# Performance work log

Hardware: AMD Instinct MI355X
Metric: run time of the kernel (lower is better)

Reference implementation:

```python
import jax, jax.numpy as jnp
import numpy as np
from jax.ops import segment_sum

N_NODES = 100000
N_EDGES = 3200000
N_GRAPHS = 64


def gcn_conv(x, src, dst, W, b, num_nodes):
    h = x @ W  # [N, H]
    loop = jnp.arange(num_nodes, dtype=src.dtype)
    s = jnp.concatenate([src, loop])
    d = jnp.concatenate([dst, loop])
    deg = segment_sum(jnp.ones_like(d, dtype=h.dtype), d, num_segments=num_nodes)
    dinv = jnp.where(deg > 0, jax.lax.rsqrt(deg), 0.0)
    norm = dinv[s] * dinv[d]  # [E+N]
    msgs = h[s] * norm[:, None]  # gather + scale
    out = segment_sum(msgs, d, num_segments=num_nodes)  # scatter-add to targets
    return out + b


def setup_inputs() -> dict:
    key = jax.random.key(0)
    ks = jax.random.split(key, 8)
    F_IN, H, C = 128, 256, 2
    x = jax.random.normal(ks[0], (N_NODES, F_IN), dtype=jnp.float32)
    edge_index = jax.random.randint(ks[1], (2, N_EDGES), 0, N_NODES, dtype=jnp.int64)
    batch = jnp.sort(jax.random.randint(ks[2], (N_NODES,), 0, N_GRAPHS, dtype=jnp.int64))
    W1 = jax.random.normal(ks[3], (F_IN, H), dtype=jnp.float32) / np.sqrt(F_IN)
    b1 = jnp.zeros((H,), dtype=jnp.float32)
    W2 = jax.random.normal(ks[4], (H, H), dtype=jnp.float32) / np.sqrt(H)
    b2 = jnp.zeros((H,), dtype=jnp.float32)
    fc_w = jax.random.normal(ks[5], (H, C), dtype=jnp.float32) / np.sqrt(H)
    fc_b = jnp.zeros((C,), dtype=jnp.float32)
    return {"x": x, "edge_index": edge_index, "batch": batch, "W1": W1, "b1": b1,
            "W2": W2, "b2": b2, "fc_w": fc_w, "fc_b": fc_b}


def reference(x, edge_index, batch, W1, b1, W2, b2, fc_w, fc_b):
    src, dst = edge_index[0], edge_index[1]
    n = x.shape[0]
    h = jax.nn.relu(gcn_conv(x, src, dst, W1, b1, n))
    h = jax.nn.relu(gcn_conv(h, src, dst, W2, b2, n))
    # global_mean_pool over graph ids
    sums = segment_sum(h, batch, num_segments=N_GRAPHS)  # [G, H]
    cnts = segment_sum(jnp.ones((n,), dtype=h.dtype), batch, num_segments=N_GRAPHS)
    pooled = sums / jnp.maximum(cnts, 1.0)[:, None]
    logits = pooled @ fc_w + fc_b
    return jax.nn.log_softmax(logits, axis=1)
```

## Files before the change

### kernel.cpp

```cpp
#include <hip/hip_runtime.h>
#include <cstdint>

#define N_NODES 100000
#define N_EDGES 3200000
#define N_GRAPHS 64
#define HDIM 256
#define F_IN 128

#define BUCKET_BITS 7
#define NPB 128
#define N_BUCKETS ((N_NODES + NPB - 1) / NPB)
#define CHUNK 8192
#define NCHUNK ((N_EDGES + CHUNK - 1) / CHUNK)

typedef __attribute__((ext_vector_type(8))) short bf16x8;
typedef __attribute__((ext_vector_type(4))) float f32x4;
typedef __attribute__((ext_vector_type(2))) float f32x2;

__device__ __forceinline__ unsigned short f2bf(float f) {
    unsigned int b = __float_as_uint(f);
    b = (b + 0x7FFFu + ((b >> 16) & 1u)) >> 16;
    return (unsigned short)b;
}
__device__ __forceinline__ float bf2f(unsigned short u) {
    return __uint_as_float((unsigned int)u << 16);
}

__device__ __forceinline__ unsigned int pack4_fp8(float a, float b, float c, float d) {
    int v = 0;
    v = __builtin_amdgcn_cvt_pk_fp8_f32(a, b, v, false);
    v = __builtin_amdgcn_cvt_pk_fp8_f32(c, d, v, true);
    return (unsigned int)v;
}
__device__ __forceinline__ unsigned char pack1_fp8(float a) {
    int v = __builtin_amdgcn_cvt_pk_fp8_f32(a, a, 0, false);
    return (unsigned char)(v & 0xFF);
}

__global__ void zero_f(float* p, int n) {
    int i = blockIdx.x * blockDim.x + threadIdx.x;
    if (i < n) p[i] = 0.0f;
}

__global__ __launch_bounds__(256) void block_count(const int* __restrict__ dst,
                                                   int* __restrict__ counts, int nE) {
    __shared__ int hist[N_BUCKETS];
    int blk = blockIdx.x, t = threadIdx.x;
    for (int i = t; i < N_BUCKETS; i += 256) hist[i] = 0;
    __syncthreads();
    int lo = blk * CHUNK;
    int hi = lo + CHUNK < nE ? lo + CHUNK : nE;
    for (int i = lo + t; i < hi; i += 256) atomicAdd(&hist[dst[i] >> BUCKET_BITS], 1);
    __syncthreads();
    for (int i = t; i < N_BUCKETS; i += 256) counts[blk * N_BUCKETS + i] = hist[i];
}

__global__ __launch_bounds__(256) void bucket_totals(const int* __restrict__ counts,
                                                     int* __restrict__ tot) {
    __shared__ int red[256];
    int b = blockIdx.x, t = threadIdx.x;
    int s = 0;
    for (int blk = t; blk < NCHUNK; blk += 256) s += counts[blk * N_BUCKETS + b];
    red[t] = s;
    __syncthreads();
    for (int o = 128; o > 0; o >>= 1) {
        if (t < o) red[t] += red[t + o];
        __syncthreads();
    }
    if (t == 0) tot[b] = red[0];
}

__global__ __launch_bounds__(1024) void scan_buckets(const int* __restrict__ tot,
                                                     int* __restrict__ base, int nb) {
    __shared__ int lds[1024];
    int t = threadIdx.x;
    int v = (t < nb) ? tot[t] : 0;
    lds[t] = v;
    __syncthreads();
    for (int off = 1; off < 1024; off <<= 1) {
        int a = (t >= off) ? lds[t - off] : 0;
        __syncthreads();
        lds[t] += a;
        __syncthreads();
    }
    int excl = lds[t] - v;
    if (t < nb) base[t] = excl;
    if (t == nb) base[t] = excl;
}

__global__ __launch_bounds__(512) void column_scan(const int* __restrict__ counts,
                                                   const int* __restrict__ base,
                                                   int* __restrict__ offs) {
    __shared__ int lds[512];
    int b = blockIdx.x, t = threadIdx.x;
    int v = (t < NCHUNK) ? counts[t * N_BUCKETS + b] : 0;
    lds[t] = v;
    __syncthreads();
    for (int off = 1; off < 512; off <<= 1) {
        int a = (t >= off) ? lds[t - off] : 0;
        __syncthreads();
        lds[t] += a;
        __syncthreads();
    }
    if (t < NCHUNK) offs[t * N_BUCKETS + b] = base[b] + lds[t] - v;
}

__global__ __launch_bounds__(256) void block_scatter(const int* __restrict__ src,
                                                     const int* __restrict__ dst,
                                                     const int* __restrict__ offs,
                                                     unsigned int* __restrict__ rec, int nE) {
    __shared__ int cur[N_BUCKETS];
    int blk = blockIdx.x, t = threadIdx.x;
    for (int i = t; i < N_BUCKETS; i += 256) cur[i] = offs[blk * N_BUCKETS + i];
    __syncthreads();
    int lo = blk * CHUNK;
    int hi = lo + CHUNK < nE ? lo + CHUNK : nE;
    for (int i = lo + t; i < hi; i += 256) {
        int d = dst[i];
        int b = d >> BUCKET_BITS;
        int pos = atomicAdd(&cur[b], 1);
        rec[pos] = (unsigned int)src[i] | ((unsigned int)(d & (NPB - 1)) << 17);
    }
}

__global__ __launch_bounds__(512) void bucket_csr(const unsigned int* __restrict__ rec,
                                                  const int* __restrict__ base,
                                                  int* __restrict__ ptr, float* __restrict__ dinv,
                                                  int* __restrict__ csr_src, int n) {
    __shared__ int hist[NPB];
    __shared__ int sc[NPB];
    __shared__ int cur[NPB];
    int b = blockIdx.x;
    int lo = base[b], hi = base[b + 1];
    int t = threadIdx.x;
    if (t < NPB) hist[t] = 0;
    __syncthreads();
    for (int i = lo + t; i < hi; i += 512) atomicAdd(&hist[rec[i] >> 17], 1);
    __syncthreads();
    if (t < NPB) sc[t] = hist[t];
    __syncthreads();
    for (int off = 1; off < NPB; off <<= 1) {
        int a = (t < NPB && t >= off) ? sc[t - off] : 0;
        __syncthreads();
        if (t < NPB) sc[t] += a;
        __syncthreads();
    }
    if (t < NPB) {
        int node = b * NPB + t;
        int incl = sc[t];
        int excl = incl - hist[t];
        if (node < n) {
            ptr[node] = lo + incl;
            dinv[node] = rsqrtf((float)hist[t] + 1.0f);
        }
        cur[t] = lo + excl;
    }
    __syncthreads();
    for (int i = lo + t; i < hi; i += 512) {
        unsigned int r = rec[i];
        int pos = atomicAdd(&cur[r >> 17], 1);
        csr_src[pos] = (int)(r & 0x1FFFFu);
    }
}

__global__ void convert_x_pre(const float* __restrict__ x, const float* __restrict__ dinv,
                              unsigned int* __restrict__ xp, int n) {
    int tid = blockIdx.x * blockDim.x + threadIdx.x;
    if (tid >= n * (F_IN / 4)) return;
    int node = tid / (F_IN / 4);
    float di = dinv[node];
    float4 v = ((const float4*)x)[tid];
    xp[tid] = pack4_fp8(v.x * di, v.y * di, v.z * di, v.w * di);
}

__global__ void pack_w(const float* __restrict__ W, unsigned short* __restrict__ hi,
                       unsigned short* __restrict__ lo, int K) {
    int idx = blockIdx.x * blockDim.x + threadIdx.x;
    if (idx >= K * HDIM) return;
    int k = idx >> 8, c = idx & 255;
    float w = W[idx];
    unsigned short h = f2bf(w);
    float hf = __uint_as_float((unsigned int)h << 16);
    unsigned short l = f2bf(w - hf);
    int pos = ((k >> 5) * 16 + (c >> 4)) * 512 + ((((k >> 3) & 3) * 16) + (c & 15)) * 8 + (k & 7);
    hi[pos] = h;
    lo[pos] = l;
}

__global__ void csr_agg128_fp8(const unsigned char* __restrict__ h, const int* __restrict__ ptr,
                               const int* __restrict__ csr, const float* __restrict__ dinv,
                               unsigned short* __restrict__ out, int n) {
    int wave = threadIdx.x >> 6, lane = threadIdx.x & 63;
    int node = blockIdx.x * 4 + wave;
    if (node >= n) return;
    int begin = node ? ptr[node - 1] : 0;
    int end = ptr[node];
    unsigned int u = *(const unsigned short*)(h + (size_t)node * 128 + lane * 2);
    f32x2 a01 = __builtin_amdgcn_cvt_pk_f32_fp8((int)u, false);
    int i = begin;
    for (; i + 16 <= end; i += 16) {
        unsigned int uu[16];
#pragma unroll
        for (int j = 0; j < 16; j++) {
            int s = csr[i + j];
            uu[j] = *(const unsigned short*)(h + (size_t)s * 128 + lane * 2);
        }
#pragma unroll
        for (int j = 0; j < 16; j++)
            a01 += __builtin_amdgcn_cvt_pk_f32_fp8((int)uu[j], false);
    }
    for (; i + 4 <= end; i += 4) {
        unsigned int uu[4];
#pragma unroll
        for (int j = 0; j < 4; j++) {
            int s = csr[i + j];
            uu[j] = *(const unsigned short*)(h + (size_t)s * 128 + lane * 2);
        }
#pragma unroll
        for (int j = 0; j < 4; j++)
            a01 += __builtin_amdgcn_cvt_pk_f32_fp8((int)uu[j], false);
    }
    for (; i < end; i++) {
        int s = csr[i];
        unsigned int u0 = *(const unsigned short*)(h + (size_t)s * 128 + lane * 2);
        a01 += __builtin_amdgcn_cvt_pk_f32_fp8((int)u0, false);
    }
    float dn = dinv[node];
    unsigned int o = (unsigned int)f2bf(a01.x * dn) | ((unsigned int)f2bf(a01.y * dn) << 16);
    *(unsigned int*)(out + (size_t)node * 128 + lane * 2) = o;
}

__global__ void csr_agg256_fp8(const unsigned char* __restrict__ h, const int* __restrict__ ptr,
                               const int* __restrict__ csr, const float* __restrict__ dinv,
                               unsigned short* __restrict__ out, int n) {
    int wave = threadIdx.x >> 6, lane = threadIdx.x & 63;
    int node = blockIdx.x * 4 + wave;
    if (node >= n) return;
    int begin = node ? ptr[node - 1] : 0;
    int end = ptr[node];
    unsigned int u = *(const unsigned int*)(h + (size_t)node * 256 + lane * 4);
    f32x2 a01 = __builtin_amdgcn_cvt_pk_f32_fp8((int)u, false);
    f32x2 a23 = __builtin_amdgcn_cvt_pk_f32_fp8((int)u, true);
    int i = begin;
    for (; i + 16 <= end; i += 16) {
        unsigned int uu[16];
#pragma unroll
        for (int j = 0; j < 16; j++) {
            int s = csr[i + j];
            uu[j] = *(const unsigned int*)(h + (size_t)s * 256 + lane * 4);
        }
#pragma unroll
        for (int j = 0; j < 16; j++) {
            a01 += __builtin_amdgcn_cvt_pk_f32_fp8((int)uu[j], false);
            a23 += __builtin_amdgcn_cvt_pk_f32_fp8((int)uu[j], true);
        }
    }
    for (; i + 4 <= end; i += 4) {
        unsigned int uu[4];
#pragma unroll
        for (int j = 0; j < 4; j++) {
            int s = csr[i + j];
            uu[j] = *(const unsigned int*)(h + (size_t)s * 256 + lane * 4);
        }
#pragma unroll
        for (int j = 0; j < 4; j++) {
            a01 += __builtin_amdgcn_cvt_pk_f32_fp8((int)uu[j], false);
            a23 += __builtin_amdgcn_cvt_pk_f32_fp8((int)uu[j], true);
        }
    }
    for (; i < end; i++) {
        int s = csr[i];
        unsigned int u0 = *(const unsigned int*)(h + (size_t)s * 256 + lane * 4);
        a01 += __builtin_amdgcn_cvt_pk_f32_fp8((int)u0, false);
        a23 += __builtin_amdgcn_cvt_pk_f32_fp8((int)u0, true);
    }
    float dn = dinv[node];
    uint2 o;
    o.x = (unsigned int)f2bf(a01.x * dn) | ((unsigned int)f2bf(a01.y * dn) << 16);
    o.y = (unsigned int)f2bf(a23.x * dn) | ((unsigned int)f2bf(a23.y * dn) << 16);
    *(uint2*)(out + (size_t)node * 256 + lane * 4) = o;
}

template <int K, int MODE>
__global__ __launch_bounds__(256, 3) void gemm_mfma(
    const unsigned short* __restrict__ A, const unsigned short* __restrict__ Whi,
    const unsigned short* __restrict__ Wlo, const float* __restrict__ bias,
    const float* __restrict__ dinv, void* __restrict__ outp, int n) {
    int wave = threadIdx.x >> 6, lane = threadIdx.x & 63;
    int quad = lane >> 4, l16 = lane & 15;
    int rowgrp = wave >> 1, colhalf = wave & 1;
    int rowbase = blockIdx.x * 64 + rowgrp * 32;

    f32x4 acc[2][8];
#pragma unroll
    for (int s = 0; s < 2; s++)
#pragma unroll
        for (int ct = 0; ct < 8; ct++) acc[s][ct] = (f32x4){0.f, 0.f, 0.f, 0.f};

    int r0 = rowbase + l16;
    int r1 = rowbase + 16 + l16;
    int rc0 = r0 < n ? r0 : n - 1;
    int rc1 = r1 < n ? r1 : n - 1;

    for (int kt = 0; kt < K / 32; kt++) {
        bf16x8 a0 = *(const bf16x8*)(A + (size_t)rc0 * K + kt * 32 + quad * 8);
        bf16x8 a1 = *(const bf16x8*)(A + (size_t)rc1 * K + kt * 32 + quad * 8);
        const unsigned short* wh = Whi + ((size_t)kt * 16 + colhalf * 8) * 512 + lane * 8;
        const unsigned short* wl = Wlo + ((size_t)kt * 16 + colhalf * 8) * 512 + lane * 8;
#pragma unroll
        for (int ct = 0; ct < 8; ct++) {
            bf16x8 bh = *(const bf16x8*)(wh + ct * 512);
            bf16x8 bl = *(const bf16x8*)(wl + ct * 512);
            acc[0][ct] = __builtin_amdgcn_mfma_f32_16x16x32_bf16(a0, bh, acc[0][ct], 0, 0, 0);
            acc[0][ct] = __builtin_amdgcn_mfma_f32_16x16x32_bf16(a0, bl, acc[0][ct], 0, 0, 0);
            acc[1][ct] = __builtin_amdgcn_mfma_f32_16x16x32_bf16(a1, bh, acc[1][ct], 0, 0, 0);
            acc[1][ct] = __builtin_amdgcn_mfma_f32_16x16x32_bf16(a1, bl, acc[1][ct], 0, 0, 0);
        }
    }

#pragma unroll
    for (int s = 0; s < 2; s++) {
#pragma unroll
        for (int ct = 0; ct < 8; ct++) {
            int col = colhalf * 128 + ct * 16 + l16;
            float b = bias[col];
#pragma unroll
            for (int r = 0; r < 4; r++) {
                int row = rowbase + s * 16 + quad * 4 + r;
                if (row < n) {
                    float v = acc[s][ct][r] + b;
                    v = v > 0.0f ? v : 0.0f;
                    if (MODE == 0) {
                        ((unsigned char*)outp)[(size_t)row * HDIM + col] = pack1_fp8(v * dinv[row]);
                    } else {
                        ((unsigned short*)outp)[(size_t)row * HDIM + col] = f2bf(v);
                    }
                }
            }
        }
    }
}

__global__ void pool_sum_runs(const unsigned short* __restrict__ h, const int* __restrict__ batch,
                              float* __restrict__ pool, int n) {
    constexpr int ROWS = 128;
    int f = threadIdx.x;
    int r0 = blockIdx.x * ROWS;
    int rend = r0 + ROWS;
    if (rend > n) rend = n;
    float acc = 0.0f;
    int cur = batch[r0];
    for (int r = r0; r < rend; r++) {
        int g = batch[r];
        if (g != cur) {
            atomicAdd(&pool[cur * HDIM + f], acc);
            acc = 0.0f; cur = g;
        }
        acc += bf2f(h[(size_t)r * HDIM + f]);
    }
    atomicAdd(&pool[cur * HDIM + f], acc);
}

__global__ void final_head(const float* __restrict__ pool, const int* __restrict__ batch,
                           const float* __restrict__ fcw, const float* __restrict__ fcb,
                           float* __restrict__ out, int n) {
    int g = threadIdx.x;
    if (g < N_GRAPHS) {
        int lo = 0, hi = n;
        while (lo < hi) { int m = (lo + hi) >> 1; if (batch[m] < g) lo = m + 1; else hi = m; }
        int b0 = lo;
        lo = 0; hi = n;
        while (lo < hi) { int m = (lo + hi) >> 1; if (batch[m] < g + 1) lo = m + 1; else hi = m; }
        int c = lo - b0;
        float cf = c > 1 ? (float)c : 1.0f;
        float inv = 1.0f / cf;
        float l0 = fcb[0], l1 = fcb[1];
        for (int f = 0; f < HDIM; f++) {
            float p = pool[g * HDIM + f] * inv;
            l0 += p * fcw[f * 2 + 0];
            l1 += p * fcw[f * 2 + 1];
        }
        float m = fmaxf(l0, l1);
        float lse = m + logf(expf(l0 - m) + expf(l1 - m));
        out[g * 2 + 0] = l0 - lse;
        out[g * 2 + 1] = l1 - lse;
    }
}

extern "C" void kernel_launch(void* const* d_in, const int* in_sizes, int n_in,
                              void* d_out, int out_size, void* d_ws, size_t ws_size,
                              hipStream_t stream) {
    const float* x = (const float*)d_in[0];
    const int* ei = (const int*)d_in[1];
    const int* batch = (const int*)d_in[2];
    const float* W1 = (const float*)d_in[3];
    const float* b1 = (const float*)d_in[4];
    const float* W2 = (const float*)d_in[5];
    const float* b2 = (const float*)d_in[6];
    const float* fcw = (const float*)d_in[7];
    const float* fcb = (const float*)d_in[8];
    float* out = (float*)d_out;

    const int* src = ei;
    const int* dst = ei + N_EDGES;

    char* ws = (char*)d_ws;
    float* dinv = (float*)ws;            ws += 4 * ((N_NODES + 255) & ~255);
    int* ptr = (int*)ws;                 ws += 4 * ((N_NODES + 255) & ~255);
    int* csr_src = (int*)ws;             ws += 4 * (size_t)N_EDGES;
    int* counts = (int*)ws;              ws += 4 * (size_t)NCHUNK * N_BUCKETS;
    int* offs = (int*)ws;                ws += 4 * (size_t)NCHUNK * N_BUCKETS;
    int* tot = (int*)ws;                 ws += 4 * 1024;
    int* bbase = (int*)ws;               ws += 4 * 1024;
    unsigned short* W1hi = (unsigned short*)ws; ws += 2 * F_IN * HDIM;
    unsigned short* W1lo = (unsigned short*)ws; ws += 2 * F_IN * HDIM;
    unsigned short* W2hi = (unsigned short*)ws; ws += 2 * HDIM * HDIM;
    unsigned short* W2lo = (unsigned short*)ws; ws += 2 * HDIM * HDIM;
    float* pool = (float*)ws;            ws += 4 * N_GRAPHS * HDIM;
    char* R0 = ws;                       ws += 4 * (size_t)N_NODES * HDIM;
    unsigned char* x_pre = (unsigned char*)R0;
    unsigned short* A1 = (unsigned short*)(R0 + (size_t)N_NODES * F_IN);
    unsigned char* h1_pre = (unsigned char*)(R0 + 3 * (size_t)N_NODES * F_IN);
    unsigned short* h2 = (unsigned short*)R0;
    unsigned short* A2 = (unsigned short*)ws;
    unsigned int* records = (unsigned int*)A2;

    block_count<<<NCHUNK, 256, 0, stream>>>(dst, counts, N_EDGES);
    bucket_totals<<<N_BUCKETS, 256, 0, stream>>>(counts, tot);
    scan_buckets<<<1, 1024, 0, stream>>>(tot, bbase, N_BUCKETS);
    column_scan<<<N_BUCKETS, 512, 0, stream>>>(counts, bbase, offs);
    block_scatter<<<NCHUNK, 256, 0, stream>>>(src, dst, offs, records, N_EDGES);
    bucket_csr<<<N_BUCKETS, 512, 0, stream>>>(records, bbase, ptr, dinv, csr_src, N_NODES);

    convert_x_pre<<<(N_NODES * (F_IN / 4) + 255) / 256, 256, 0, stream>>>(
        x, dinv, (unsigned int*)x_pre, N_NODES);
    pack_w<<<(F_IN * HDIM + 255) / 256, 256, 0, stream>>>(W1, W1hi, W1lo, F_IN);
    pack_w<<<(HDIM * HDIM + 255) / 256, 256, 0, stream>>>(W2, W2hi, W2lo, HDIM);
    zero_f<<<(N_GRAPHS * HDIM + 255) / 256, 256, 0, stream>>>(pool, N_GRAPHS * HDIM);

    csr_agg128_fp8<<<(N_NODES + 3) / 4, 256, 0, stream>>>(x_pre, ptr, csr_src, dinv, A1, N_NODES);
    gemm_mfma<F_IN, 0><<<(N_NODES + 63) / 64, 256, 0, stream>>>(A1, W1hi, W1lo, b1, dinv,
                                                                h1_pre, N_NODES);
    csr_agg256_fp8<<<(N_NODES + 3) / 4, 256, 0, stream>>>(h1_pre, ptr, csr_src, dinv, A2, N_NODES);
    gemm_mfma<HDIM, 2><<<(N_NODES + 63) / 64, 256, 0, stream>>>(A2, W2hi, W2lo, b2, dinv,
                                                                h2, N_NODES);

    pool_sum_runs<<<(N_NODES + 127) / 128, 256, 0, stream>>>(h2, batch, pool, N_NODES);
    final_head<<<1, 64, 0, stream>>>(pool, batch, fcw, fcb, out, N_NODES);
}
```

Baseline: 650.8 us.

## Slice CSR aggregation by feature columns with edge-parallel lanes and shuffle reduce

```diff
diff --git a/kernel.cpp b/kernel.cpp
--- a/kernel.cpp
+++ b/kernel.cpp
@@ -187,80 +187,43 @@
     lo[pos] = l;
 }
 
-__global__ void csr_agg128_fp8(const unsigned char* __restrict__ h, const int* __restrict__ ptr,
-                               const int* __restrict__ csr, const float* __restrict__ dinv,
-                               unsigned short* __restrict__ out, int n) {
+template <int F>
+__global__ __launch_bounds__(256) void csr_agg_sliced(
+    const unsigned char* __restrict__ h, const int* __restrict__ ptr,
+    const int* __restrict__ csr, const float* __restrict__ dinv,
+    unsigned short* __restrict__ out, int n) {
+    constexpr int NSLICES = F / 32;
+    constexpr int NODEGRP = 8 / NSLICES;
+    int slot = blockIdx.x & 7;
+    int nodeblk = blockIdx.x >> 3;
     int wave = threadIdx.x >> 6, lane = threadIdx.x & 63;
-    int node = blockIdx.x * 4 + wave;
+    int slice = slot % NSLICES;
+    int grp = slot / NSLICES;
+    int node = nodeblk * (4 * NODEGRP) + grp * 4 + wave;
     if (node >= n) return;
+    int eg = lane >> 3;
+    int cp = lane & 7;
+    int colbyte = slice * 32 + cp * 4;
+
     int begin = node ? ptr[node - 1] : 0;
     int end = ptr[node];
-    unsigned int u = *(const unsigned short*)(h + (size_t)node * 128 + lane * 2);
-    f32x2 a01 = __builtin_amdgcn_cvt_pk_f32_fp8((int)u, false);
-    int i = begin;
-    for (; i + 16 <= end; i += 16) {
-        unsigned int uu[16];
-#pragma unroll
-        for (int j = 0; j < 16; j++) {
-            int s = csr[i + j];
-            uu[j] = *(const unsigned short*)(h + (size_t)s * 128 + lane * 2);
-        }
-#pragma unroll
-        for (int j = 0; j < 16; j++)
-            a01 += __builtin_amdgcn_cvt_pk_f32_fp8((int)uu[j], false);
-    }
-    for (; i + 4 <= end; i += 4) {
+
+    unsigned int uown = 0;
+    if (eg == 0) uown = *(const unsigned int*)(h + (size_t)node * F + colbyte);
+    f32x2 a01 = __builtin_amdgcn_cvt_pk_f32_fp8((int)uown, false);
+    f32x2 a23 = __builtin_amdgcn_cvt_pk_f32_fp8((int)uown, true);
+
+    for (int i = begin; i < end; i += 32) {
         unsigned int uu[4];
 #pragma unroll
         for (int j = 0; j < 4; j++) {
-            int s = csr[i + j];
-            uu[j] = *(const unsigned short*)(h + (size_t)s * 128 + lane * 2);
-        }
-#pragma unroll
-        for (int j = 0; j < 4; j++)
-            a01 += __builtin_amdgcn_cvt_pk_f32_fp8((int)uu[j], false);
-    }
-    for (; i < end; i++) {
-        int s = csr[i];
-        unsigned int u0 = *(const unsigned short*)(h + (size_t)s * 128 + lane * 2);
-        a01 += __builtin_amdgcn_cvt_pk_f32_fp8((int)u0, false);
-    }
-    float dn = dinv[node];
-    unsigned int o = (unsigned int)f2bf(a01.x * dn) | ((unsigned int)f2bf(a01.y * dn) << 16);
-    *(unsigned int*)(out + (size_t)node * 128 + lane * 2) = o;
-}
-
-__global__ void csr_agg256_fp8(const unsigned char* __restrict__ h, const int* __restrict__ ptr,
-                               const int* __restrict__ csr, const float* __restrict__ dinv,
-                               unsigned short* __restrict__ out, int n) {
-    int wave = threadIdx.x >> 6, lane = threadIdx.x & 63;
-    int node = blockIdx.x * 4 + wave;
-    if (node >= n) return;
-    int begin = node ? ptr[node - 1] : 0;
-    int end = ptr[node];
-    unsigned int u = *(const unsigned int*)(h + (size_t)node * 256 + lane * 4);
-    f32x2 a01 = __builtin_amdgcn_cvt_pk_f32_fp8((int)u, false);
-    f32x2 a23 = __builtin_amdgcn_cvt_pk_f32_fp8((int)u, true);
-    int i = begin;
-    for (; i + 16 <= end; i += 16) {
-        unsigned int uu[16];
-#pragma unroll
-        for (int j = 0; j < 16; j++) {
-            int s = csr[i + j];
-            uu[j] = *(const unsigned int*)(h + (size_t)s * 256 + lane * 4);
-        }
-#pragma unroll
-        for (int j = 0; j < 16; j++) {
-            a01 += __builtin_amdgcn_cvt_pk_f32_fp8((int)uu[j], false);
-            a23 += __builtin_amdgcn_cvt_pk_f32_fp8((int)uu[j], true);
-        }
-    }
-    for (; i + 4 <= end; i += 4) {
-        unsigned int uu[4];
-#pragma unroll
-        for (int j = 0; j < 4; j++) {
-            int s = csr[i + j];
-            uu[j] = *(const unsigned int*)(h + (size_t)s * 256 + lane * 4);
+            int e = i + j * 8 + eg;
+            unsigned int u = 0;
+            if (e < end) {
+                int s = csr[e];
+                u = *(const unsigned int*)(h + (size_t)s * F + colbyte);
+            }
+            uu[j] = u;
         }
 #pragma unroll
         for (int j = 0; j < 4; j++) {
@@ -268,17 +231,22 @@
             a23 += __builtin_amdgcn_cvt_pk_f32_fp8((int)uu[j], true);
         }
     }
-    for (; i < end; i++) {
-        int s = csr[i];
-        unsigned int u0 = *(const unsigned int*)(h + (size_t)s * 256 + lane * 4);
-        a01 += __builtin_amdgcn_cvt_pk_f32_fp8((int)u0, false);
-        a23 += __builtin_amdgcn_cvt_pk_f32_fp8((int)u0, true);
-    }
-    float dn = dinv[node];
-    uint2 o;
-    o.x = (unsigned int)f2bf(a01.x * dn) | ((unsigned int)f2bf(a01.y * dn) << 16);
-    o.y = (unsigned int)f2bf(a23.x * dn) | ((unsigned int)f2bf(a23.y * dn) << 16);
-    *(uint2*)(out + (size_t)node * 256 + lane * 4) = o;
+
+#pragma unroll
+    for (int m = 8; m <= 32; m <<= 1) {
+        a01.x += __shfl_xor(a01.x, m);
+        a01.y += __shfl_xor(a01.y, m);
+        a23.x += __shfl_xor(a23.x, m);
+        a23.y += __shfl_xor(a23.y, m);
+    }
+
+    if (eg == 0) {
+        float dn = dinv[node];
+        uint2 o;
+        o.x = (unsigned int)f2bf(a01.x * dn) | ((unsigned int)f2bf(a01.y * dn) << 16);
+        o.y = (unsigned int)f2bf(a23.x * dn) | ((unsigned int)f2bf(a23.y * dn) << 16);
+        *(uint2*)(out + (size_t)node * F + slice * 32 + cp * 4) = o;
+    }
 }
 
 template <int K, int MODE>
@@ -438,10 +406,12 @@
     pack_w<<<(HDIM * HDIM + 255) / 256, 256, 0, stream>>>(W2, W2hi, W2lo, HDIM);
     zero_f<<<(N_GRAPHS * HDIM + 255) / 256, 256, 0, stream>>>(pool, N_GRAPHS * HDIM);
 
-    csr_agg128_fp8<<<(N_NODES + 3) / 4, 256, 0, stream>>>(x_pre, ptr, csr_src, dinv, A1, N_NODES);
+    csr_agg_sliced<F_IN><<<((N_NODES + 7) / 8) * 8, 256, 0, stream>>>(
+        x_pre, ptr, csr_src, dinv, A1, N_NODES);
     gemm_mfma<F_IN, 0><<<(N_NODES + 63) / 64, 256, 0, stream>>>(A1, W1hi, W1lo, b1, dinv,
                                                                 h1_pre, N_NODES);
-    csr_agg256_fp8<<<(N_NODES + 3) / 4, 256, 0, stream>>>(h1_pre, ptr, csr_src, dinv, A2, N_NODES);
+    csr_agg_sliced<HDIM><<<((N_NODES + 3) / 4) * 8, 256, 0, stream>>>(
+        h1_pre, ptr, csr_src, dinv, A2, N_NODES);
     gemm_mfma<HDIM, 2><<<(N_NODES + 63) / 64, 256, 0, stream>>>(A2, W2hi, W2lo, b2, dinv,
                                                                 h2, N_NODES);
 
```

Result: slower. 1.213 ms (+86.4%).
